# Kernel optimization log

Measured on AMD Instinct MI355X. Metric: run time of the kernel, lower is better.

Reference implementation:

```python
import jax, jax.numpy as jnp
import numpy as np

DIM = 256
HEADS = 4
DIM_HEAD = 32
HIDDEN = HEADS * DIM_HEAD  # 128
SCALE = DIM_HEAD ** -0.5
EPS = 1e-5


def setup_inputs() -> dict:
    key = jax.random.key(0)
    ks = jax.random.split(key, 6)
    B, H, W = 32, 64, 64
    x = jax.random.normal(ks[0], (B, DIM, H, W), dtype=jnp.float32)
    w_qkv = jax.random.normal(ks[1], (3 * HIDDEN, DIM), dtype=jnp.float32) * (DIM ** -0.5)
    w_out = jax.random.normal(ks[2], (DIM, HIDDEN), dtype=jnp.float32) * (HIDDEN ** -0.5)
    b_out = jnp.zeros((DIM,), dtype=jnp.float32)
    g = jnp.ones((DIM,), dtype=jnp.float32)
    b = jnp.zeros((DIM,), dtype=jnp.float32)
    return {"x": x, "w_qkv": w_qkv, "w_out": w_out, "b_out": b_out, "g": g, "b": b}


def reference(x, w_qkv, w_out, b_out, g, b):
    B, C, H, W = x.shape
    n = H * W
    # 1x1 conv qkv projection (no bias)
    qkv = jnp.einsum('oc,bchw->bohw', w_qkv, x)  # [B, 3*HIDDEN, H, W]
    qkv = qkv.reshape(B, 3, HEADS, DIM_HEAD, n)  # [B, 3, h, d, n]
    q, k, v = qkv[:, 0], qkv[:, 1], qkv[:, 2]
    q = jax.nn.softmax(q, axis=-2) * SCALE       # softmax over head dim d
    k = jax.nn.softmax(k, axis=-1)               # softmax over tokens n
    context = jnp.einsum('bhdn,bhen->bhde', k, v)
    out = jnp.einsum('bhde,bhdn->bhen', context, q)  # [B, h, e, n]
    out = out.reshape(B, HIDDEN, H, W)
    # 1x1 conv output projection with bias
    out = jnp.einsum('oc,bchw->bohw', w_out, out) + b_out[None, :, None, None]
    # LayerNorm over channel dim (biased variance)
    mean = jnp.mean(out, axis=1, keepdims=True)
    var = jnp.var(out, axis=1, keepdims=True)
    out = (out - mean) / jnp.sqrt(var + EPS) * g[None, :, None, None] + b[None, :, None, None]
    return out
```

## Files before the change

kernel.cpp:

```cpp
#include <hip/hip_runtime.h>
#include <math.h>

#define NPIX 4096
#define BATCH 32
#define CDIM 256
#define SCALE_F 0.17677669529663687f
#define EPS_F 1e-5f

typedef _Float16 f16;
typedef _Float16 f16x8 __attribute__((ext_vector_type(8)));
typedef _Float16 f16x4 __attribute__((ext_vector_type(4)));
typedef float    f32x4 __attribute__((ext_vector_type(4)));

static __device__ __forceinline__ f32x4 mfma16(f16x8 a, f16x8 b, f32x4 c) {
    return __builtin_amdgcn_mfma_f32_16x16x32_f16(a, b, c, 0, 0, 0);
}

__global__ __launch_bounds__(256)
void wconv(const float* __restrict__ w, f16* __restrict__ wh)
{
    int i = blockIdx.x * 256 + threadIdx.x;
    float4 v = ((const float4*)w)[i];
    f16x4 o = {(f16)v.x, (f16)v.y, (f16)v.z, (f16)v.w};
    int row = i >> 6;
    int k4  = (i * 4) & 255;
    *(f16x4*)&wh[(k4 >> 5) * 12288 + row * 32 + (k4 & 31)] = o;
}

__global__ __launch_bounds__(256)
void qkv_fused(const f16* __restrict__ wh, const float* __restrict__ x,
               f16* __restrict__ qhatT, float* __restrict__ ctx,
               float* __restrict__ ksum)
{
    __shared__ __align__(16) f16 As[384 * 32];
    __shared__ __align__(16) f16 Bs[64 * 32];
    __shared__ __align__(16) f16 ek_s[128 * 64];
    __shared__ __align__(16) f16 v_s[128 * 64];
    __shared__ float ksum_s[128];

    const int b = blockIdx.y;
    const int t = threadIdx.x;
    const int lane = t & 63, w = t >> 6;
    const int lane15 = lane & 15, lg = lane >> 4;
    const int grow = w * 96;

    const float* xb = x + (size_t)b * 256 * NPIX;
    f16* qT = qhatT + (size_t)b * NPIX * 128;

    const int bn = t & 63;
    const int bc = t >> 6;
    const int bsw = bn * 32 + ((bc ^ ((bn >> 1) & 3)) << 3);

    if (t < 128) ksum_s[t] = 0.f;

    f32x4 ctxacc[2][2];
    const f32x4 z4 = {0.f, 0.f, 0.f, 0.f};
    ctxacc[0][0] = z4; ctxacc[0][1] = z4; ctxacc[1][0] = z4; ctxacc[1][1] = z4;

    for (int tile = 0; tile < 4; tile++) {
        const int n0 = blockIdx.x * 256 + tile * 64;
        f32x4 acc[6][4];
        #pragma unroll
        for (int i = 0; i < 6; i++)
            #pragma unroll
            for (int j = 0; j < 4; j++) acc[i][j] = z4;

        float v8[8];
        #pragma unroll
        for (int m = 0; m < 8; m++)
            v8[m] = xb[(size_t)(bc * 8 + m) * NPIX + n0 + bn];

        for (int k0 = 0; k0 < 256; k0 += 32) {
            const f16* whp = wh + (k0 >> 5) * 12288;
            #pragma unroll
            for (int it = 0; it < 6; it++) {
                int c = t + it * 256;
                int row = c >> 2, ch = c & 3;
                *(f16x8*)&As[row * 32 + ((ch ^ ((row >> 1) & 3)) << 3)] =
                    *(const f16x8*)&whp[c * 8];
            }
            f16x8 bv;
            #pragma unroll
            for (int m = 0; m < 8; m++) bv[m] = (f16)v8[m];
            *(f16x8*)&Bs[bsw] = bv;
            __syncthreads();
            if (k0 < 224) {
                #pragma unroll
                for (int m = 0; m < 8; m++)
                    v8[m] = xb[(size_t)(k0 + 32 + bc * 8 + m) * NPIX + n0 + bn];
            }
            f16x8 af[6], bf[4];
            #pragma unroll
            for (int j = 0; j < 4; j++) {
                int rr = j * 16 + lane15;
                bf[j] = *(const f16x8*)&Bs[rr * 32 + ((lg ^ ((rr >> 1) & 3)) << 3)];
            }
            #pragma unroll
            for (int i = 0; i < 6; i++) {
                int rr = grow + i * 16 + lane15;
                af[i] = *(const f16x8*)&As[rr * 32 + ((lg ^ ((rr >> 1) & 3)) << 3)];
            }
            #pragma unroll
            for (int i = 0; i < 6; i++)
                #pragma unroll
                for (int j = 0; j < 4; j++)
                    acc[i][j] = mfma16(af[i], bf[j], acc[i][j]);
            __syncthreads();
        }

        #pragma unroll
        for (int i = 0; i < 6; i++) {
            const int rbase = grow + i * 16;
            if (rbase < 128) {
                if ((rbase & 31) == 0) {
                    #pragma unroll
                    for (int j = 0; j < 4; j++) {
                        float e0[2][4]; float s = 0.f;
                        #pragma unroll
                        for (int ii = 0; ii < 2; ii++)
                            #pragma unroll
                            for (int r = 0; r < 4; r++) {
                                float ev = __expf(acc[i + ii][j][r]);
                                e0[ii][r] = ev; s += ev;
                            }
                        s += __shfl_xor(s, 16); s += __shfl_xor(s, 32);
                        float inv = SCALE_F / s;
                        int n = n0 + j * 16 + lane15;
                        #pragma unroll
                        for (int ii = 0; ii < 2; ii++) {
                            int d0 = rbase + ii * 16 + lg * 4;
                            f16x4 pk;
                            #pragma unroll
                            for (int r = 0; r < 4; r++) pk[r] = (f16)(e0[ii][r] * inv);
                            *(f16x4*)(qT + (size_t)n * 128 + d0) = pk;
                        }
                    }
                }
            } else if (rbase < 256) {
                const int kb = rbase - 128;
                #pragma unroll
                for (int r = 0; r < 4; r++) {
                    int row = kb + lg * 4 + r;
                    float p = 0.f;
                    #pragma unroll
                    for (int j = 0; j < 4; j++) {
                        float ev = __expf(acc[i][j][r]);
                        p += ev;
                        int col = j * 16 + lane15;
                        ek_s[row * 64 + ((((col >> 3) ^ (row & 7)) << 3) | (col & 7))] =
                            (f16)ev;
                    }
                    p += __shfl_xor(p, 1); p += __shfl_xor(p, 2);
                    p += __shfl_xor(p, 4); p += __shfl_xor(p, 8);
                    if (lane15 == 0) atomicAdd(&ksum_s[row], p);
                }
            } else {
                const int vb = rbase - 256;
                #pragma unroll
                for (int r = 0; r < 4; r++) {
                    int row = vb + lg * 4 + r;
                    #pragma unroll
                    for (int j = 0; j < 4; j++) {
                        int col = j * 16 + lane15;
                        v_s[row * 64 + ((((col >> 3) ^ (row & 7)) << 3) | (col & 7))] =
                            (f16)acc[i][j][r];
                    }
                }
            }
        }
        __syncthreads();
        #pragma unroll
        for (int ks2 = 0; ks2 < 2; ks2++) {
            f16x8 a2[2], b2[2];
            #pragma unroll
            for (int i2 = 0; i2 < 2; i2++) {
                int row = w * 32 + i2 * 16 + lane15;
                int off = row * 64 + (((ks2 * 4 + lg) ^ (row & 7)) << 3);
                a2[i2] = *(const f16x8*)&ek_s[off];
                b2[i2] = *(const f16x8*)&v_s[off];
            }
            #pragma unroll
            for (int i2 = 0; i2 < 2; i2++)
                #pragma unroll
                for (int j2 = 0; j2 < 2; j2++)
                    ctxacc[i2][j2] = mfma16(a2[i2], b2[j2], ctxacc[i2][j2]);
        }
    }

    if (t < 128) atomicAdd(&ksum[b * 128 + t], ksum_s[t]);

    float* cg = ctx + ((size_t)b * 4 + w) * 1024;
    #pragma unroll
    for (int i2 = 0; i2 < 2; i2++)
        #pragma unroll
        for (int j2 = 0; j2 < 2; j2++)
            #pragma unroll
            for (int r = 0; r < 4; r++)
                atomicAdd(&cg[(i2 * 16 + lg * 4 + r) * 32 + j2 * 16 + lane15],
                          ctxacc[i2][j2][r]);
}

__global__ __launch_bounds__(256)
void weff_kernel(const float* __restrict__ wout, const float* __restrict__ ctx,
                 const float* __restrict__ ksum, f16* __restrict__ weff)
{
    const int bh = blockIdx.x;
    const int b = bh >> 2, h = bh & 3;
    __shared__ float cs[1024];
    __shared__ float inv_s[32];
    const int t = threadIdx.x;
    for (int i = t; i < 1024; i += 256) cs[i] = ctx[(size_t)bh * 1024 + i];
    if (t < 32) inv_s[t] = 1.f / ksum[b * 128 + h * 32 + t];
    __syncthreads();
    float acc[32] = {};
    const float* wrow = wout + (size_t)t * 128 + h * 32;
    for (int e = 0; e < 32; e++) {
        float wv = wrow[e];
        #pragma unroll
        for (int d = 0; d < 32; d++) acc[d] += wv * cs[d * 32 + e];
    }
    f16* wo = weff + ((size_t)b * 256 + t) * 128 + h * 32;
    #pragma unroll
    for (int d = 0; d < 32; d++) wo[d] = (f16)(acc[d] * inv_s[d]);
}

__global__ __launch_bounds__(256)
void out_mfma_ln(const f16* __restrict__ weff, const f16* __restrict__ qhatT,
                 const float* __restrict__ bias, const float* __restrict__ g,
                 const float* __restrict__ bb, float* __restrict__ out)
{
    __shared__ __align__(16) f16 As2[256 * 32];
    __shared__ __align__(16) f16 Bs2[128 * 32];
    __shared__ float pb[256], pg[256], pbb[256];
    __shared__ float lds_s[4][128], lds_s2[4][128];
    const int b = blockIdx.y;
    const int tileN = blockIdx.x * 128;
    const int t = threadIdx.x;
    const int lane = t & 63, w = t >> 6;
    const int lane15 = lane & 15, lg = lane >> 4;
    pb[t] = bias[t]; pg[t] = g[t]; pbb[t] = bb[t];
    const f16* Aw = weff + (size_t)b * 256 * 128;
    const f16* Bw = qhatT + (size_t)b * NPIX * 128;
    f32x4 acc[4][8];
    const f32x4 z4 = {0.f, 0.f, 0.f, 0.f};
    #pragma unroll
    for (int i = 0; i < 4; i++)
        #pragma unroll
        for (int j = 0; j < 8; j++) acc[i][j] = z4;

    for (int k0 = 0; k0 < 128; k0 += 32) {
        #pragma unroll
        for (int it = 0; it < 4; it++) {
            int c = t + it * 256;
            int row = c >> 2, koff = (c & 3) * 8;
            *(f16x8*)&As2[row * 32 + koff] = *(const f16x8*)&Aw[(size_t)row * 128 + k0 + koff];
        }
        #pragma unroll
        for (int it = 0; it < 2; it++) {
            int c = t + it * 256;
            int row = c >> 2, koff = (c & 3) * 8;
            *(f16x8*)&Bs2[row * 32 + koff] =
                *(const f16x8*)&Bw[(size_t)(tileN + row) * 128 + k0 + koff];
        }
        __syncthreads();
        f16x8 af[4], bf[8];
        #pragma unroll
        for (int i = 0; i < 4; i++)
            af[i] = *(const f16x8*)&As2[(w * 64 + i * 16 + lane15) * 32 + lg * 8];
        #pragma unroll
        for (int j = 0; j < 8; j++)
            bf[j] = *(const f16x8*)&Bs2[(j * 16 + lane15) * 32 + lg * 8];
        #pragma unroll
        for (int i = 0; i < 4; i++)
            #pragma unroll
            for (int j = 0; j < 8; j++)
                acc[i][j] = mfma16(af[i], bf[j], acc[i][j]);
        __syncthreads();
    }
    #pragma unroll
    for (int i = 0; i < 4; i++)
        #pragma unroll
        for (int r = 0; r < 4; r++) {
            float bo = pb[w * 64 + i * 16 + lg * 4 + r];
            #pragma unroll
            for (int j = 0; j < 8; j++) acc[i][j][r] += bo;
        }
    #pragma unroll
    for (int j = 0; j < 8; j++) {
        float s = 0.f, s2 = 0.f;
        #pragma unroll
        for (int i = 0; i < 4; i++)
            #pragma unroll
            for (int r = 0; r < 4; r++) { float v = acc[i][j][r]; s += v; s2 += v * v; }
        s += __shfl_xor(s, 16);  s += __shfl_xor(s, 32);
        s2 += __shfl_xor(s2, 16); s2 += __shfl_xor(s2, 32);
        if (lg == 0) { lds_s[w][j * 16 + lane15] = s; lds_s2[w][j * 16 + lane15] = s2; }
    }
    __syncthreads();
    float mean[8], rstd[8];
    #pragma unroll
    for (int j = 0; j < 8; j++) {
        int col = j * 16 + lane15;
        float S = lds_s[0][col] + lds_s[1][col] + lds_s[2][col] + lds_s[3][col];
        float S2 = lds_s2[0][col] + lds_s2[1][col] + lds_s2[2][col] + lds_s2[3][col];
        float mn = S * (1.f / 256.f);
        mean[j] = mn;
        rstd[j] = rsqrtf(S2 * (1.f / 256.f) - mn * mn + EPS_F);
    }
    float* ob = out + (size_t)b * CDIM * NPIX;
    #pragma unroll
    for (int i = 0; i < 4; i++)
        #pragma unroll
        for (int r = 0; r < 4; r++) {
            int row = w * 64 + i * 16 + lg * 4 + r;
            float gm = pg[row], bt = pbb[row];
            #pragma unroll
            for (int j = 0; j < 8; j++)
                ob[(size_t)row * NPIX + tileN + j * 16 + lane15] =
                    (acc[i][j][r] - mean[j]) * rstd[j] * gm + bt;
        }
}

extern "C" void kernel_launch(void* const* d_in, const int* in_sizes, int n_in,
                              void* d_out, int out_size, void* d_ws, size_t ws_size,
                              hipStream_t stream)
{
    const float* x     = (const float*)d_in[0];
    const float* w_qkv = (const float*)d_in[1];
    const float* w_out = (const float*)d_in[2];
    const float* b_out = (const float*)d_in[3];
    const float* g     = (const float*)d_in[4];
    const float* bvec  = (const float*)d_in[5];
    float* out = (float*)d_out;

    char* wsb = (char*)d_ws;
    f16*   qhatT = (f16*)wsb;
    float* ctx   = (float*)(wsb + 33554432);
    float* ksum  = (float*)(wsb + 34078720);
    f16*   weff  = (f16*)(wsb + 34095104);
    f16*   wh    = (f16*)(wsb + 36192256);

    hipMemsetAsync(ctx, 0, 540672, stream);
    wconv<<<96, 256, 0, stream>>>(w_qkv, wh);
    qkv_fused<<<dim3(16, BATCH), 256, 0, stream>>>(wh, x, qhatT, ctx, ksum);
    weff_kernel<<<128, 256, 0, stream>>>(w_out, ctx, ksum, weff);
    out_mfma_ln<<<dim3(32, BATCH), 256, 0, stream>>>(weff, qhatT, b_out, g, bvec, out);
}
```

Before: 412.3 us.

## Pre-transpose x to fp16 token-major layout in two batch halves

Adds a transpose kernel that converts x to fp16 in [n][k] layout, so the QKV GEMM loads one 16-byte vector per thread instead of eight strided scalar fp32 loads. The batch is processed in two halves of 16 to bound the workspace, and qkv_fused now uses 128-token blocks across 32 x-blocks. The weight conversion keeps plain row-major layout and is indexed directly. The cost is an extra pass that writes and rereads x in fp16, plus more kernel launches.

```diff
diff --git a/kernel.cpp b/kernel.cpp
--- a/kernel.cpp
+++ b/kernel.cpp
@@ -22,13 +22,39 @@
     int i = blockIdx.x * 256 + threadIdx.x;
     float4 v = ((const float4*)w)[i];
     f16x4 o = {(f16)v.x, (f16)v.y, (f16)v.z, (f16)v.w};
-    int row = i >> 6;
-    int k4  = (i * 4) & 255;
-    *(f16x4*)&wh[(k4 >> 5) * 12288 + row * 32 + (k4 & 31)] = o;
-}
-
-__global__ __launch_bounds__(256)
-void qkv_fused(const f16* __restrict__ wh, const float* __restrict__ x,
+    ((f16x4*)wh)[i] = o;
+}
+
+__global__ __launch_bounds__(256)
+void transpose_x(const float* __restrict__ x, f16* __restrict__ xt, int b0)
+{
+    __shared__ f16 T[64][66];
+    const int b = b0 + blockIdx.z;
+    const int n0 = blockIdx.x * 64, k0 = blockIdx.y * 64;
+    const float* xb = x + ((size_t)b * 256 + k0) * NPIX + n0;
+    const int t = threadIdx.x;
+    const int kl = t >> 2;
+    #pragma unroll
+    for (int it = 0; it < 4; it++) {
+        int nq = (t & 3) + it * 4;
+        float4 v = *(const float4*)&xb[(size_t)kl * NPIX + nq * 4];
+        T[kl][nq * 4 + 0] = (f16)v.x;
+        T[kl][nq * 4 + 1] = (f16)v.y;
+        T[kl][nq * 4 + 2] = (f16)v.z;
+        T[kl][nq * 4 + 3] = (f16)v.w;
+    }
+    __syncthreads();
+    const int nl = t >> 2, kc = t & 3;
+    f16 tmp[16];
+    #pragma unroll
+    for (int j = 0; j < 16; j++) tmp[j] = T[kc * 16 + j][nl];
+    f16* dst = xt + ((size_t)blockIdx.z * NPIX + n0 + nl) * 256 + k0 + kc * 16;
+    *(f16x8*)dst = *(f16x8*)&tmp[0];
+    *(f16x8*)(dst + 8) = *(f16x8*)&tmp[8];
+}
+
+__global__ __launch_bounds__(256)
+void qkv_fused(const f16* __restrict__ wh, const f16* __restrict__ xt, int b0,
                f16* __restrict__ qhatT, float* __restrict__ ctx,
                float* __restrict__ ksum)
 {
@@ -38,13 +64,14 @@
     __shared__ __align__(16) f16 v_s[128 * 64];
     __shared__ float ksum_s[128];
 
-    const int b = blockIdx.y;
+    const int z = blockIdx.y;
+    const int b = b0 + z;
     const int t = threadIdx.x;
     const int lane = t & 63, w = t >> 6;
     const int lane15 = lane & 15, lg = lane >> 4;
     const int grow = w * 96;
 
-    const float* xb = x + (size_t)b * 256 * NPIX;
+    const f16* xtb = xt + (size_t)z * NPIX * 256;
     f16* qT = qhatT + (size_t)b * NPIX * 128;
 
     const int bn = t & 63;
@@ -57,38 +84,28 @@
     const f32x4 z4 = {0.f, 0.f, 0.f, 0.f};
     ctxacc[0][0] = z4; ctxacc[0][1] = z4; ctxacc[1][0] = z4; ctxacc[1][1] = z4;
 
-    for (int tile = 0; tile < 4; tile++) {
-        const int n0 = blockIdx.x * 256 + tile * 64;
+    for (int tile = 0; tile < 2; tile++) {
+        const int n0 = blockIdx.x * 128 + tile * 64;
         f32x4 acc[6][4];
         #pragma unroll
         for (int i = 0; i < 6; i++)
             #pragma unroll
             for (int j = 0; j < 4; j++) acc[i][j] = z4;
 
-        float v8[8];
-        #pragma unroll
-        for (int m = 0; m < 8; m++)
-            v8[m] = xb[(size_t)(bc * 8 + m) * NPIX + n0 + bn];
+        f16x8 bv = *(const f16x8*)&xtb[(size_t)(n0 + bn) * 256 + bc * 8];
 
         for (int k0 = 0; k0 < 256; k0 += 32) {
-            const f16* whp = wh + (k0 >> 5) * 12288;
             #pragma unroll
             for (int it = 0; it < 6; it++) {
                 int c = t + it * 256;
                 int row = c >> 2, ch = c & 3;
                 *(f16x8*)&As[row * 32 + ((ch ^ ((row >> 1) & 3)) << 3)] =
-                    *(const f16x8*)&whp[c * 8];
-            }
-            f16x8 bv;
-            #pragma unroll
-            for (int m = 0; m < 8; m++) bv[m] = (f16)v8[m];
+                    *(const f16x8*)&wh[(size_t)row * 256 + k0 + ch * 8];
+            }
             *(f16x8*)&Bs[bsw] = bv;
             __syncthreads();
-            if (k0 < 224) {
-                #pragma unroll
-                for (int m = 0; m < 8; m++)
-                    v8[m] = xb[(size_t)(k0 + 32 + bc * 8 + m) * NPIX + n0 + bn];
-            }
+            if (k0 < 224)
+                bv = *(const f16x8*)&xtb[(size_t)(n0 + bn) * 256 + k0 + 32 + bc * 8];
             f16x8 af[6], bf[4];
             #pragma unroll
             for (int j = 0; j < 4; j++) {
@@ -334,15 +351,20 @@
     float* out = (float*)d_out;
 
     char* wsb = (char*)d_ws;
-    f16*   qhatT = (f16*)wsb;
-    float* ctx   = (float*)(wsb + 33554432);
-    float* ksum  = (float*)(wsb + 34078720);
-    f16*   weff  = (f16*)(wsb + 34095104);
-    f16*   wh    = (f16*)(wsb + 36192256);
+    f16*   xt    = (f16*)wsb;
+    f16*   qhatT = (f16*)(wsb + 33554432);
+    float* ctx   = (float*)(wsb + 67108864);
+    float* ksum  = (float*)(wsb + 67633152);
+    f16*   weff  = (f16*)(wsb + 67649536);
+    f16*   wh    = (f16*)(wsb + 69746688);
 
     hipMemsetAsync(ctx, 0, 540672, stream);
     wconv<<<96, 256, 0, stream>>>(w_qkv, wh);
-    qkv_fused<<<dim3(16, BATCH), 256, 0, stream>>>(wh, x, qhatT, ctx, ksum);
+    for (int p = 0; p < 2; p++) {
+        transpose_x<<<dim3(64, 4, 16), 256, 0, stream>>>(x, xt, p * 16);
+        qkv_fused<<<dim3(32, 16), 256, 0, stream>>>(wh, xt, p * 16,
+                                                    qhatT, ctx, ksum);
+    }
     weff_kernel<<<128, 256, 0, stream>>>(w_out, ctx, ksum, weff);
     out_mfma_ln<<<dim3(32, BATCH), 256, 0, stream>>>(weff, qhatT, b_out, g, bvec, out);
 }
```

Result: slower. 452.1 us (+9.7%).
